# Optimization experiments

Measured on AMD Instinct MI355X. Metric: run time of the kernel, lower is better.

The kernel has to match this reference:

```python
import jax, jax.numpy as jnp
import numpy as np

BS, C_IN, CTX, TGT = 2, 8, 1024, 96
D_MODEL, N_HEADS, D_FF, N_LAYERS = 256, 16, 1024, 4
PF, SF, PC, SC = 8, 4, 32, 16
NF = (CTX + SF - PF) // SF + 1   # 256 fine patches (incl. end-pad)
NC = (CTX + SC - PC) // SC + 1   # 64 coarse patches
TOTAL = NF + NC                  # 320
EPS = 1e-5
DK = D_MODEL // N_HEADS
SCALE = DK ** -0.5


def _patchify(z, plen, stride):
    # ReplicationPad1d((0, stride)) then unfold -> (bs, c, n_patches, plen)
    pad = jnp.broadcast_to(z[..., -1:], z.shape[:-1] + (stride,))
    zp = jnp.concatenate([z, pad], axis=-1)
    n = (zp.shape[-1] - plen) // stride + 1
    idx = np.arange(n)[:, None] * stride + np.arange(plen)[None, :]
    return zp[..., idx]


def _layernorm(x, s, b):
    m = x.mean(-1, keepdims=True)
    v = jnp.var(x, axis=-1, keepdims=True)
    return (x - m) * jax.lax.rsqrt(v + EPS) * s + b


def setup_inputs() -> dict:
    key = jax.random.key(0)
    ks = jax.random.split(key, 16)
    g = lambda k, shape: jax.random.normal(k, shape, jnp.float32) * 0.02
    return {
        "z": jax.random.normal(ks[0], (BS, C_IN, CTX), jnp.float32),
        "revin_w": jnp.ones((C_IN,), jnp.float32),
        "revin_b": jnp.zeros((C_IN,), jnp.float32),
        "Wf": g(ks[1], (PF, D_MODEL)), "bf": jnp.zeros((D_MODEL,), jnp.float32),
        "Wc": g(ks[2], (PC, D_MODEL)), "bc": jnp.zeros((D_MODEL,), jnp.float32),
        "W_pos": jax.random.uniform(ks[3], (TOTAL, D_MODEL), jnp.float32, -0.02, 0.02),
        "WQ": g(ks[4], (N_LAYERS, D_MODEL, D_MODEL)), "bQ": jnp.zeros((N_LAYERS, D_MODEL), jnp.float32),
        "WK": g(ks[5], (N_LAYERS, D_MODEL, D_MODEL)), "bK": jnp.zeros((N_LAYERS, D_MODEL), jnp.float32),
        "WV": g(ks[6], (N_LAYERS, D_MODEL, D_MODEL)), "bV": jnp.zeros((N_LAYERS, D_MODEL), jnp.float32),
        "WO": g(ks[7], (N_LAYERS, D_MODEL, D_MODEL)), "bO": jnp.zeros((N_LAYERS, D_MODEL), jnp.float32),
        "ln1_s": jnp.ones((N_LAYERS, D_MODEL), jnp.float32), "ln1_b": jnp.zeros((N_LAYERS, D_MODEL), jnp.float32),
        "ln2_s": jnp.ones((N_LAYERS, D_MODEL), jnp.float32), "ln2_b": jnp.zeros((N_LAYERS, D_MODEL), jnp.float32),
        "F1": g(ks[8], (N_LAYERS, D_MODEL, D_FF)), "c1": jnp.zeros((N_LAYERS, D_FF), jnp.float32),
        "F2": g(ks[9], (N_LAYERS, D_FF, D_MODEL)), "c2": jnp.zeros((N_LAYERS, D_MODEL), jnp.float32),
        "Wh": g(ks[10], (D_MODEL * TOTAL, TGT)), "bh": jnp.zeros((TGT,), jnp.float32),
    }


def reference(z, revin_w, revin_b, Wf, bf, Wc, bc, W_pos, WQ, bQ, WK, bK, WV, bV,
              WO, bO, ln1_s, ln1_b, ln2_s, ln2_b, F1, c1, F2, c2, Wh, bh):
    # RevIN norm over the time axis (last axis of (bs, c, T))
    mean = z.mean(-1, keepdims=True)
    std = jnp.sqrt(jnp.var(z, axis=-1, keepdims=True) + EPS)
    zn = (z - mean) / std * revin_w[None, :, None] + revin_b[None, :, None]

    # dual-scale patch embedding
    x_fine = _patchify(zn, PF, SF) @ Wf + bf      # (bs, c, NF, d)
    x_coarse = _patchify(zn, PC, SC) @ Wc + bc    # (bs, c, NC, d)
    x = jnp.concatenate([x_fine, x_coarse], axis=2)  # (bs, c, TOTAL, d)

    u = x.reshape(BS * C_IN, TOTAL, D_MODEL) + W_pos  # (B, S, d), B=bs*c

    # residual-score transformer encoder (post-norm)
    prev = None
    for l in range(N_LAYERS):
        q = (u @ WQ[l] + bQ[l]).reshape(-1, TOTAL, N_HEADS, DK).transpose(0, 2, 1, 3)
        k = (u @ WK[l] + bK[l]).reshape(-1, TOTAL, N_HEADS, DK).transpose(0, 2, 1, 3)
        v = (u @ WV[l] + bV[l]).reshape(-1, TOTAL, N_HEADS, DK).transpose(0, 2, 1, 3)
        s = jnp.einsum('bhqd,bhkd->bhqk', q, k) * SCALE
        if prev is not None:
            s = s + prev
        w = jax.nn.softmax(s, axis=-1)
        o = jnp.einsum('bhqk,bhkd->bhqd', w, v).transpose(0, 2, 1, 3).reshape(-1, TOTAL, D_MODEL)
        o = o @ WO[l] + bO[l]
        u = _layernorm(u + o, ln1_s[l], ln1_b[l])
        h = jax.nn.gelu(u @ F1[l] + c1[l], approximate=False) @ F2[l] + c2[l]
        u = _layernorm(u + h, ln2_s[l], ln2_b[l])
        prev = s

    # head: (bs, c, TOTAL, d) -> permute -> flatten(d, TOTAL) -> linear
    zz = u.reshape(BS, C_IN, TOTAL, D_MODEL).transpose(0, 1, 3, 2).reshape(BS, C_IN, D_MODEL * TOTAL)
    out = zz @ Wh + bh  # (bs, c, TGT)

    # RevIN denorm
    out = (out - revin_b[None, :, None]) / (revin_w[None, :, None] + EPS * EPS) * std + mean
    return out
```

## Files before the change

kernel.cpp:

```cpp
#include <hip/hip_runtime.h>
#include <math.h>

typedef unsigned short ushort;
typedef unsigned int uint;
typedef __attribute__((ext_vector_type(8))) short short8;
typedef __attribute__((ext_vector_type(4))) float f32x4;
typedef __attribute__((ext_vector_type(4))) ushort us4;

constexpr int BS = 2, C_IN = 8, CTX = 1024, TGT = 96;
constexpr int DM = 256, NH = 16, DFF = 1024, NL = 4;
constexpr int NF = 256, TOTAL = 320;
constexpr int NB = 16;
constexpr int DK = 16;
constexpr float EPS = 1e-5f;
constexpr float SCALE = 0.25f;
constexpr int KHEAD = DM * TOTAL;
constexpr int M = NB * TOTAL;

__device__ __forceinline__ ushort f2b(float x) {
    uint u = __float_as_uint(x);
    u += 0x7fff + ((u >> 16) & 1);
    return (ushort)(u >> 16);
}
__device__ __forceinline__ float bu2f(ushort x) { return __uint_as_float(((uint)x) << 16); }
__device__ __forceinline__ uint pack2(float a, float b) { return (uint)f2b(a) | ((uint)f2b(b) << 16); }

typedef __attribute__((address_space(3))) uint lds_u32;
typedef const __attribute__((address_space(1))) uint glb_u32;
__device__ __forceinline__ void ldst16(const void* g, void* l) {
    __builtin_amdgcn_global_load_lds((glb_u32*)g, (lds_u32*)l, 16, 0, 0);
}

#define PIPE_BARRIER() asm volatile("s_waitcnt vmcnt(0)\n\ts_barrier" ::: "memory")

__global__ __launch_bounds__(256) void k_prep(
        const float* __restrict__ WQ, const float* __restrict__ WK,
        const float* __restrict__ WV, const float* __restrict__ WO,
        const float* __restrict__ F1, const float* __restrict__ F2,
        const float* __restrict__ Wh,
        ushort* __restrict__ Wtqkv, ushort* __restrict__ WtO,
        ushort* __restrict__ Ft1, ushort* __restrict__ Ft2,
        ushort* __restrict__ WhT2,
        const float* __restrict__ z, const float* __restrict__ rw,
        const float* __restrict__ rb,
        const float* __restrict__ Wf, const float* __restrict__ bfv,
        const float* __restrict__ Wc, const float* __restrict__ bcv,
        const float* __restrict__ Wpos, ushort* __restrict__ u,
        const float* __restrict__ bhv, float* __restrict__ outp,
        float* __restrict__ scalef) {
    __shared__ __align__(16) ushort tile[64 * 98];
    __shared__ float szn[CTX];
    __shared__ float red1[4], red2[4];
    int i = blockIdx.x, tid = threadIdx.x;

    if (i < 768) {
        const float* src; ushort* dst; int lsrc, ldst_, r0, c0;
        if (i < 256) {
            int mat = i >> 4, l = mat >> 2, w = mat & 3;
            src = (w == 0 ? WQ : (w == 1 ? WK : (w == 2 ? WV : WO))) + l * 65536;
            dst = (w < 3) ? (Wtqkv + (size_t)l * 768 * 256 + w * 65536)
                          : (WtO + (size_t)l * 65536);
            lsrc = 256; ldst_ = 256; r0 = ((i >> 2) & 3) * 64; c0 = (i & 3) * 64;
        } else if (i < 512) {
            int j = i - 256, l = j >> 6, t = j & 63;
            src = F1 + (size_t)l * 262144; dst = Ft1 + (size_t)l * 262144;
            lsrc = 1024; ldst_ = 256; r0 = (t >> 4) * 64; c0 = (t & 15) * 64;
        } else {
            int j = i - 512, l = j >> 6, t = j & 63;
            src = F2 + (size_t)l * 262144; dst = Ft2 + (size_t)l * 262144;
            lsrc = 256; ldst_ = 1024; r0 = (t >> 2) * 64; c0 = (t & 3) * 64;
        }
#pragma unroll
        for (int it = 0; it < 4; it++) {
            int fid = it * 256 + tid;
            int fr = fid >> 4, fc = fid & 15;
            f32x4 v = *(const f32x4*)&src[(size_t)(r0 + fr) * lsrc + c0 + fc * 4];
            ushort* tr = &tile[fr * 66];
            tr[fc * 4 + 0] = f2b(v[0]); tr[fc * 4 + 1] = f2b(v[1]);
            tr[fc * 4 + 2] = f2b(v[2]); tr[fc * 4 + 3] = f2b(v[3]);
        }
        __syncthreads();
#pragma unroll
        for (int it = 0; it < 4; it++) {
            int sid = it * 256 + tid;
            int cr = sid >> 4, cc = sid & 15;
            us4 v = (us4){ tile[(cc * 4 + 0) * 66 + cr], tile[(cc * 4 + 1) * 66 + cr],
                           tile[(cc * 4 + 2) * 66 + cr], tile[(cc * 4 + 3) * 66 + cr] };
            *(us4*)&dst[(size_t)(c0 + cr) * ldst_ + r0 + cc * 4] = v;
        }
    } else if (i < 2048) {
        int j = i - 768;
        int pp = j >> 2, d0 = (j & 3) * 64;
#pragma unroll
        for (int it = 0; it < 6; it++) {
            int fid = it * 256 + tid;
            int fr = fid / 24, fc = fid % 24;
            f32x4 v = *(const f32x4*)&Wh[((size_t)(d0 + fr) * 320 + pp) * 96 + fc * 4];
            ushort* tr = &tile[fr * 98];
            tr[fc * 4 + 0] = f2b(v[0]); tr[fc * 4 + 1] = f2b(v[1]);
            tr[fc * 4 + 2] = f2b(v[2]); tr[fc * 4 + 3] = f2b(v[3]);
        }
        __syncthreads();
#pragma unroll
        for (int it = 0; it < 6; it++) {
            int sid = it * 256 + tid;
            int tr = sid >> 4, dc = sid & 15;
            us4 v = (us4){ tile[(dc * 4 + 0) * 98 + tr], tile[(dc * 4 + 1) * 98 + tr],
                           tile[(dc * 4 + 2) * 98 + tr], tile[(dc * 4 + 3) * 98 + tr] };
            *(us4*)&WhT2[(size_t)tr * KHEAD + pp * 256 + d0 + dc * 4] = v;
        }
    } else {
        int j = i - 2048;
        int bc = j / 80, pb = j % 80;
        int wave = tid >> 6, lane = tid & 63;
        f32x4 zv = *(const f32x4*)&z[bc * CTX + tid * 4];
        float s1 = zv[0] + zv[1] + zv[2] + zv[3];
        float s2 = zv[0] * zv[0] + zv[1] * zv[1] + zv[2] * zv[2] + zv[3] * zv[3];
#pragma unroll
        for (int off = 1; off < 64; off <<= 1) {
            s1 += __shfl_xor(s1, off);
            s2 += __shfl_xor(s2, off);
        }
        if (lane == 0) { red1[wave] = s1; red2[wave] = s2; }
        __syncthreads();
        s1 = red1[0] + red1[1] + red1[2] + red1[3];
        s2 = red2[0] + red2[1] + red2[2] + red2[3];
        float m = s1 * (1.0f / CTX);
        float var = s2 * (1.0f / CTX) - m * m;
        float sd = sqrtf(var + EPS);
        int c = bc & 7;
        float w = rw[c], bb = rb[c];
        float inv_sd_w = w / sd;
#pragma unroll
        for (int k = 0; k < 4; k++) szn[tid * 4 + k] = (zv[k] - m) * inv_sd_w + bb;
        if (pb == 0) {
            if (tid < TGT) outp[bc * TGT + tid] = (bhv[tid] - bb) / (w + EPS * EPS) * sd + m;
            if (tid == 0) scalef[bc] = sd / (w + EPS * EPS);
        }
        __syncthreads();
#pragma unroll
        for (int pi = 0; pi < 4; pi++) {
            int p = pb * 4 + pi, d = tid;
            float acc;
            if (p < NF) {
                acc = bfv[d];
                int base = p * 4;
#pragma unroll
                for (int q = 0; q < 8; q++)
                    acc += szn[min(base + q, CTX - 1)] * Wf[q * DM + d];
            } else {
                acc = bcv[d];
                int base = (p - NF) * 16;
#pragma unroll
                for (int q = 0; q < 32; q++)
                    acc += szn[min(base + q, CTX - 1)] * Wc[q * DM + d];
            }
            acc += Wpos[p * DM + d];
            u[((size_t)bc * TOTAL + p) * DM + d] = f2b(acc);
        }
    }
}

template <int GELU, int QKV>
__global__ __launch_bounds__(256) void k_gemm_mfma(const ushort* __restrict__ A,
                                                   const ushort* __restrict__ Wt,
                                                   const float* __restrict__ b0,
                                                   const float* __restrict__ b1,
                                                   const float* __restrict__ b2,
                                                   ushort* __restrict__ C,
                                                   ushort* __restrict__ C2,
                                                   int Mm, int N, int K) {
    __shared__ ushort As[2][64][32];
    __shared__ ushort Bs[2][64][32];
    int tid = threadIdx.x;
    int wave = tid >> 6, lane = tid & 63;
    int quad = lane >> 4, l16 = lane & 15;
    int m0 = blockIdx.y * 64, n0 = blockIdx.x * 64;

    f32x4 acc[4];
#pragma unroll
    for (int nt = 0; nt < 4; nt++) acc[nt] = (f32x4){0.f, 0.f, 0.f, 0.f};

    int srow = wave * 16 + (lane >> 2);
    int sc = (lane & 3) ^ ((srow >> 1) & 3);
    const ushort* Ag = &A[(size_t)(m0 + srow) * K + sc * 8];
    const ushort* Bg = &Wt[(size_t)(n0 + srow) * K + sc * 8];
    int rchunk = (quad ^ ((l16 >> 1) & 3)) * 8;

    ldst16(Ag, &As[0][wave * 16][0]);
    ldst16(Bg, &Bs[0][wave * 16][0]);
    PIPE_BARRIER();

    int nstep = K >> 5;
    int cur = 0;
    for (int t = 0; t < nstep; t++) {
        if (t + 1 < nstep) {
            ldst16(Ag + (t + 1) * 32, &As[cur ^ 1][wave * 16][0]);
            ldst16(Bg + (t + 1) * 32, &Bs[cur ^ 1][wave * 16][0]);
        }
        short8 af = *(const short8*)&As[cur][wave * 16 + l16][rchunk];
#pragma unroll
        for (int nt = 0; nt < 4; nt++) {
            short8 bf = *(const short8*)&Bs[cur][nt * 16 + l16][rchunk];
            acc[nt] = __builtin_amdgcn_mfma_f32_16x16x32_bf16(af, bf, acc[nt], 0, 0, 0);
        }
        PIPE_BARRIER();
        cur ^= 1;
    }
#pragma unroll
    for (int nt = 0; nt < 4; nt++) {
        int col = n0 + nt * 16 + l16;
        float bi;
        if (QKV) {
            int bs = (n0 + nt * 16) >> 8;
            const float* bp = bs == 0 ? b0 : (bs == 1 ? b1 : b2);
            bi = bp[col & 255];
        } else {
            bi = b0[col];
        }
#pragma unroll
        for (int r = 0; r < 4; r++) {
            int rowm = m0 + wave * 16 + quad * 4 + r;
            float vv = acc[nt][r] + bi;
            if (GELU) vv = vv * 0.5f * (1.0f + erff(vv * 0.70710678118f));
            if (QKV) {
                int bs = col >> 8;
                ushort* dst = (bs == 2) ? (C2 + (size_t)rowm * DM)
                                        : (C + (size_t)bs * (M * DM) + (size_t)rowm * DM);
                dst[col & 255] = f2b(vv);
            } else {
                C[(size_t)rowm * N + col] = f2b(vv);
            }
        }
    }
}

__global__ __launch_bounds__(256) void k_gemm_ln16(const ushort* __restrict__ A,
                                                   const ushort* __restrict__ Wt,
                                                   const float* __restrict__ bias,
                                                   const float* __restrict__ ls,
                                                   const float* __restrict__ lb,
                                                   ushort* __restrict__ u, int K) {
    __shared__ ushort As[2][16][32];
    __shared__ ushort Bs[2][256][32];
    __shared__ float ps1[16][4], ps2[16][4];
    int tid = threadIdx.x;
    int wave = tid >> 6, lane = tid & 63;
    int quad = lane >> 4, l16 = lane & 15;
    int m0 = blockIdx.x * 16;

    f32x4 acc[4];
#pragma unroll
    for (int nt = 0; nt < 4; nt++) acc[nt] = (f32x4){0.f, 0.f, 0.f, 0.f};

    int brow = wave * 16 + (lane >> 2);
    int bc_swz = (lane & 3) ^ ((brow >> 1) & 3);
    const ushort* Bg0 = &Wt[(size_t)brow * K + bc_swz * 8];
    int ar = lane >> 2;
    int ac = (lane & 3) ^ ((ar >> 1) & 3);
    const ushort* Ag = &A[(size_t)(m0 + ar) * K + ac * 8];
    int rchunk = (quad ^ ((l16 >> 1) & 3)) * 8;

    if (tid < 64) ldst16(Ag, &As[0][0][0]);
#pragma unroll
    for (int i = 0; i < 4; i++)
        ldst16(Bg0 + (size_t)i * 64 * K, &Bs[0][i * 64 + wave * 16][0]);
    PIPE_BARRIER();

    int nstep = K >> 5;
    int cur = 0;
    for (int t = 0; t < nstep; t++) {
        if (t + 1 < nstep) {
            if (tid < 64) ldst16(Ag + (t + 1) * 32, &As[cur ^ 1][0][0]);
#pragma unroll
            for (int i = 0; i < 4; i++)
                ldst16(Bg0 + (size_t)i * 64 * K + (t + 1) * 32, &Bs[cur ^ 1][i * 64 + wave * 16][0]);
        }
        short8 af = *(const short8*)&As[cur][l16][rchunk];
#pragma unroll
        for (int nt = 0; nt < 4; nt++) {
            short8 bf = *(const short8*)&Bs[cur][wave * 64 + nt * 16 + l16][rchunk];
            acc[nt] = __builtin_amdgcn_mfma_f32_16x16x32_bf16(af, bf, acc[nt], 0, 0, 0);
        }
        PIPE_BARRIER();
        cur ^= 1;
    }
    float xv[4][4];
#pragma unroll
    for (int r = 0; r < 4; r++) {
        int rowg = m0 + quad * 4 + r;
        float s1 = 0.f, s2 = 0.f;
#pragma unroll
        for (int nt = 0; nt < 4; nt++) {
            int col = wave * 64 + nt * 16 + l16;
            float x = acc[nt][r] + bias[col] + bu2f(u[(size_t)rowg * DM + col]);
            xv[r][nt] = x; s1 += x; s2 += x * x;
        }
        s1 += __shfl_xor(s1, 1); s2 += __shfl_xor(s2, 1);
        s1 += __shfl_xor(s1, 2); s2 += __shfl_xor(s2, 2);
        s1 += __shfl_xor(s1, 4); s2 += __shfl_xor(s2, 4);
        s1 += __shfl_xor(s1, 8); s2 += __shfl_xor(s2, 8);
        if (l16 == 0) { ps1[quad * 4 + r][wave] = s1; ps2[quad * 4 + r][wave] = s2; }
    }
    __syncthreads();
#pragma unroll
    for (int r = 0; r < 4; r++) {
        int rowl = quad * 4 + r, rowg = m0 + rowl;
        float s1 = ps1[rowl][0] + ps1[rowl][1] + ps1[rowl][2] + ps1[rowl][3];
        float s2 = ps2[rowl][0] + ps2[rowl][1] + ps2[rowl][2] + ps2[rowl][3];
        float m = s1 * (1.0f / DM);
        float var = s2 * (1.0f / DM) - m * m;
        float rs = rsqrtf(var + EPS);
#pragma unroll
        for (int nt = 0; nt < 4; nt++) {
            int col = wave * 64 + nt * 16 + l16;
            u[(size_t)rowg * DM + col] = f2b((xv[r][nt] - m) * rs * ls[col] + lb[col]);
        }
    }
}

__global__ __launch_bounds__(256, 4) void k_attn(const ushort* __restrict__ qk, const ushort* __restrict__ vm,
                                                 ushort* __restrict__ ao, int nj) {
    __shared__ ushort sh[15360];
    uint* sh32 = (uint*)sh;
    int bh = blockIdx.x, b = bh >> 4, h = bh & 15;
    int i0 = blockIdx.y * 64;
    int t = threadIdx.x, wave = t >> 6, lane = t & 63, quad = lane >> 4, l16 = lane & 15;
    const short8 zero8 = (short8){0, 0, 0, 0, 0, 0, 0, 0};

    f32x4 acc[20];
#pragma unroll
    for (int nt = 0; nt < 20; nt++) acc[nt] = (f32x4){0.f, 0.f, 0.f, 0.f};

    for (int idx = t; idx < 320; idx += 256) {
        int jp = idx >> 1, dh = idx & 1;
        int j = jp * 2;
        uint4 a = *(const uint4*)&vm[((size_t)b * TOTAL + j) * DM + h * DK + dh * 8];
        uint4 bb = *(const uint4*)&vm[((size_t)b * TOTAL + j + 1) * DM + h * DK + dh * 8];
        const ushort* ap = (const ushort*)&a;
        const ushort* bp = (const ushort*)&bb;
        int jr = j & 31;
        int q = (jr & 15) >> 2, jj = ((jr >> 4) << 2) + (jr & 3);
        int base = 10240 + ((j >> 5) * 4 + q) * 128 + jj;
#pragma unroll
        for (int dd = 0; dd < 8; dd++) {
            int d = dh * 8 + dd;
            uint val = (uint)ap[dd] | ((uint)bp[dd] << 16);
            sh32[(base + d * 8) >> 1] = val;
        }
    }

    for (int jl = 0; jl < nj; jl++) {
        const ushort* qm = qk + (size_t)(2 * jl) * M * DM;
        const ushort* km = qm + (size_t)M * DM;
        int kb = (jl & 1) * 5120;
        for (int idx = t; idx < 640; idx += 256) {
            int j = idx >> 1, half = idx & 1;
            short8 kv = *(const short8*)&km[((size_t)b * TOTAL + j) * DM + h * DK + half * 8];
            int jt = j >> 4, jln = j & 15;
            *(short8*)&sh[kb + ((jt * 2 + half) * 16 + jln) * 8] = kv;
        }
        short8 qf = zero8;
        if (quad < 2) qf = *(const short8*)&qm[((size_t)b * TOTAL + i0 + wave * 16 + l16) * DM + h * DK + quad * 8];
        __syncthreads();
#pragma unroll
        for (int nt = 0; nt < 20; nt++) {
            short8 kf = *(const short8*)&sh[kb + ((nt * 2 + (quad & 1)) * 16 + l16) * 8];
            acc[nt] = __builtin_amdgcn_mfma_f32_16x16x32_bf16(kf, qf, acc[nt], 0, 0, 0);
        }
    }

    float mx = -1e30f;
#pragma unroll
    for (int nt = 0; nt < 20; nt++)
#pragma unroll
        for (int r = 0; r < 4; r++) { acc[nt][r] *= SCALE; mx = fmaxf(mx, acc[nt][r]); }
    mx = fmaxf(mx, __shfl_xor(mx, 16));
    mx = fmaxf(mx, __shfl_xor(mx, 32));
    float sum = 0.f;
#pragma unroll
    for (int nt = 0; nt < 20; nt++)
#pragma unroll
        for (int r = 0; r < 4; r++) { acc[nt][r] = __expf(acc[nt][r] - mx); sum += acc[nt][r]; }
    sum += __shfl_xor(sum, 16);
    sum += __shfl_xor(sum, 32);
    float inv = 1.f / sum;
#pragma unroll
    for (int nt = 0; nt < 20; nt++)
#pragma unroll
        for (int r = 0; r < 4; r++) acc[nt][r] *= inv;

    f32x4 oacc = (f32x4){0.f, 0.f, 0.f, 0.f};
#pragma unroll
    for (int jt2 = 0; jt2 < 10; jt2++) {
        short8 vt = *(const short8*)&sh[10240 + ((jt2 * 4 + quad) * 16 + l16) * 8];
        union { short8 v; uint u[4]; } pf;
        pf.u[0] = pack2(acc[2 * jt2][0], acc[2 * jt2][1]);
        pf.u[1] = pack2(acc[2 * jt2][2], acc[2 * jt2][3]);
        pf.u[2] = pack2(acc[2 * jt2 + 1][0], acc[2 * jt2 + 1][1]);
        pf.u[3] = pack2(acc[2 * jt2 + 1][2], acc[2 * jt2 + 1][3]);
        oacc = __builtin_amdgcn_mfma_f32_16x16x32_bf16(vt, pf.v, oacc, 0, 0, 0);
    }
    us4 ov4 = (us4){f2b(oacc[0]), f2b(oacc[1]), f2b(oacc[2]), f2b(oacc[3])};
    *(us4*)&ao[((size_t)b * TOTAL + i0 + wave * 16 + l16) * DM + h * DK + quad * 4] = ov4;
}

__global__ __launch_bounds__(256) void k_head(const ushort* __restrict__ u, const ushort* __restrict__ WhT2,
                                              const float* __restrict__ scalef, float* __restrict__ out) {
    int t0 = blockIdx.x * 16;
    int wave = threadIdx.x >> 6, lane = threadIdx.x & 63;
    int quad = lane >> 4, l16 = lane & 15;
    int chunk = blockIdx.y * 4 + wave;
    int kbeg = chunk * 1024;
    f32x4 acc = (f32x4){0.f, 0.f, 0.f, 0.f};
    const ushort* za = &u[(size_t)l16 * KHEAD + quad * 8];
    const ushort* wb = &WhT2[(size_t)(t0 + l16) * KHEAD + quad * 8];
#pragma unroll 4
    for (int k = kbeg; k < kbeg + 1024; k += 32) {
        short8 af = *(const short8*)&za[k];
        short8 bf = *(const short8*)&wb[k];
        acc = __builtin_amdgcn_mfma_f32_16x16x32_bf16(af, bf, acc, 0, 0, 0);
    }
#pragma unroll
    for (int r = 0; r < 4; r++) {
        int bcr = quad * 4 + r;
        atomicAdd(&out[bcr * TGT + t0 + l16], acc[r] * scalef[bcr]);
    }
}

extern "C" void kernel_launch(void* const* d_in, const int* in_sizes, int n_in,
                              void* d_out, int out_size, void* d_ws, size_t ws_size,
                              hipStream_t stream) {
    const float* z       = (const float*)d_in[0];
    const float* revin_w = (const float*)d_in[1];
    const float* revin_b = (const float*)d_in[2];
    const float* Wf      = (const float*)d_in[3];
    const float* bfv     = (const float*)d_in[4];
    const float* Wc      = (const float*)d_in[5];
    const float* bcv     = (const float*)d_in[6];
    const float* Wpos    = (const float*)d_in[7];
    const float* WQ      = (const float*)d_in[8];
    const float* bQ      = (const float*)d_in[9];
    const float* WK      = (const float*)d_in[10];
    const float* bK      = (const float*)d_in[11];
    const float* WV      = (const float*)d_in[12];
    const float* bV      = (const float*)d_in[13];
    const float* WO      = (const float*)d_in[14];
    const float* bO      = (const float*)d_in[15];
    const float* ln1s    = (const float*)d_in[16];
    const float* ln1b    = (const float*)d_in[17];
    const float* ln2s    = (const float*)d_in[18];
    const float* ln2b    = (const float*)d_in[19];
    const float* F1      = (const float*)d_in[20];
    const float* c1      = (const float*)d_in[21];
    const float* F2      = (const float*)d_in[22];
    const float* c2      = (const float*)d_in[23];
    const float* Wh      = (const float*)d_in[24];
    const float* bh      = (const float*)d_in[25];
    float* out = (float*)d_out;

    char* p = (char*)d_ws;
    float* scalef = (float*)p;   p += 16 * 4;
    p = (char*)(((size_t)p + 255) & ~255ull);
    ushort* u     = (ushort*)p;  p += (size_t)M * DM * 2;
    ushort* qkbuf = (ushort*)p;  p += (size_t)NL * 2 * M * DM * 2;
    ushort* vbuf  = (ushort*)p;  p += (size_t)M * DM * 2;
    ushort* ax    = (ushort*)p;  p += (size_t)M * DM * 2;
    ushort* hbuf  = (ushort*)p;  p += (size_t)M * DFF * 2;
    ushort* Wtqkv = (ushort*)p;  p += (size_t)NL * 768 * 256 * 2;
    ushort* WtO   = (ushort*)p;  p += (size_t)NL * 256 * 256 * 2;
    ushort* Ft1   = (ushort*)p;  p += (size_t)NL * 1024 * 256 * 2;
    ushort* Ft2   = (ushort*)p;  p += (size_t)NL * 256 * 1024 * 2;
    ushort* WhT2  = (ushort*)p;  p += (size_t)TGT * KHEAD * 2;

    k_prep<<<3328, 256, 0, stream>>>(WQ, WK, WV, WO, F1, F2, Wh,
                                     Wtqkv, WtO, Ft1, Ft2, WhT2,
                                     z, revin_w, revin_b,
                                     Wf, bfv, Wc, bcv, Wpos, u,
                                     bh, out, scalef);

    for (int l = 0; l < NL; l++) {
        k_gemm_mfma<0, 1><<<dim3(12, 80), 256, 0, stream>>>(
            u, Wtqkv + (size_t)l * 768 * 256, bQ + l * DM, bK + l * DM, bV + l * DM,
            qkbuf + (size_t)l * 2 * M * DM, vbuf, M, 768, 256);
        k_attn<<<dim3(NB * NH, 5), 256, 0, stream>>>(qkbuf, vbuf, ax, l + 1);
        k_gemm_ln16<<<M / 16, 256, 0, stream>>>(
            ax, WtO + (size_t)l * 65536, bO + l * DM, ln1s + l * DM, ln1b + l * DM, u, 256);
        k_gemm_mfma<1, 0><<<dim3(16, 80), 256, 0, stream>>>(
            u, Ft1 + (size_t)l * 262144, c1 + l * DFF, c1, c1, hbuf, hbuf, M, 1024, 256);
        k_gemm_ln16<<<M / 16, 256, 0, stream>>>(
            hbuf, Ft2 + (size_t)l * 262144, c2 + l * DM, ln2s + l * DM, ln2b + l * DM, u, 1024);
    }

    k_head<<<dim3(TGT / 16, 20), 256, 0, stream>>>(u, WhT2, scalef, out);
}
```

Baseline: 441.4 us.

## Triple-buffer LDS in MFMA GEMM kernels with partial vmcnt waits

Both the generic MFMA GEMM and the GEMM+LayerNorm kernel move from double to triple-buffered LDS staging. Loads run two K-steps ahead, and the wait at each step uses a partial vmcnt count instead of draining every outstanding load. This hides more global-load latency behind the MFMAs. In exchange it uses more LDS per block, and it relies on exact vmcnt counts per wave, which differ for wave 0 because it issues the extra A loads.

```diff
diff --git a/kernel.cpp b/kernel.cpp
--- a/kernel.cpp
+++ b/kernel.cpp
@@ -31,7 +31,9 @@
     __builtin_amdgcn_global_load_lds((glb_u32*)g, (lds_u32*)l, 16, 0, 0);
 }
 
-#define PIPE_BARRIER() asm volatile("s_waitcnt vmcnt(0)\n\ts_barrier" ::: "memory")
+#define WAITV(n) asm volatile("s_waitcnt vmcnt(" #n ")" ::: "memory")
+#define SBAR()   asm volatile("s_barrier" ::: "memory")
+#define SBARW()  asm volatile("s_waitcnt lgkmcnt(0)\n\ts_barrier" ::: "memory")
 
 __global__ __launch_bounds__(256) void k_prep(
         const float* __restrict__ WQ, const float* __restrict__ WK,
@@ -170,8 +172,8 @@
                                                    ushort* __restrict__ C,
                                                    ushort* __restrict__ C2,
                                                    int Mm, int N, int K) {
-    __shared__ ushort As[2][64][32];
-    __shared__ ushort Bs[2][64][32];
+    __shared__ ushort As[3][64][32];
+    __shared__ ushort Bs[3][64][32];
     int tid = threadIdx.x;
     int wave = tid >> 6, lane = tid & 63;
     int quad = lane >> 4, l16 = lane & 15;
@@ -187,25 +189,32 @@
     const ushort* Bg = &Wt[(size_t)(n0 + srow) * K + sc * 8];
     int rchunk = (quad ^ ((l16 >> 1) & 3)) * 8;
 
-    ldst16(Ag, &As[0][wave * 16][0]);
-    ldst16(Bg, &Bs[0][wave * 16][0]);
-    PIPE_BARRIER();
-
     int nstep = K >> 5;
+    ldst16(Ag,      &As[0][wave * 16][0]);
+    ldst16(Bg,      &Bs[0][wave * 16][0]);
+    ldst16(Ag + 32, &As[1][wave * 16][0]);
+    ldst16(Bg + 32, &Bs[1][wave * 16][0]);
+    ldst16(Ag + 64, &As[2][wave * 16][0]);
+    ldst16(Bg + 64, &Bs[2][wave * 16][0]);
+
     int cur = 0;
     for (int t = 0; t < nstep; t++) {
-        if (t + 1 < nstep) {
-            ldst16(Ag + (t + 1) * 32, &As[cur ^ 1][wave * 16][0]);
-            ldst16(Bg + (t + 1) * 32, &Bs[cur ^ 1][wave * 16][0]);
-        }
+        if (t < nstep - 2) WAITV(4);
+        else if (t == nstep - 2) WAITV(2);
+        else WAITV(0);
+        SBAR();
         short8 af = *(const short8*)&As[cur][wave * 16 + l16][rchunk];
 #pragma unroll
         for (int nt = 0; nt < 4; nt++) {
             short8 bf = *(const short8*)&Bs[cur][nt * 16 + l16][rchunk];
             acc[nt] = __builtin_amdgcn_mfma_f32_16x16x32_bf16(af, bf, acc[nt], 0, 0, 0);
         }
-        PIPE_BARRIER();
-        cur ^= 1;
+        if (t + 3 < nstep) {
+            SBARW();
+            ldst16(Ag + (t + 3) * 32, &As[cur][wave * 16][0]);
+            ldst16(Bg + (t + 3) * 32, &Bs[cur][wave * 16][0]);
+        }
+        cur = (cur == 2) ? 0 : cur + 1;
     }
 #pragma unroll
     for (int nt = 0; nt < 4; nt++) {
@@ -241,8 +250,8 @@
                                                    const float* __restrict__ ls,
                                                    const float* __restrict__ lb,
                                                    ushort* __restrict__ u, int K) {
-    __shared__ ushort As[2][16][32];
-    __shared__ ushort Bs[2][256][32];
+    __shared__ ushort As[3][16][32];
+    __shared__ ushort Bs[3][256][32];
     __shared__ float ps1[16][4], ps2[16][4];
     int tid = threadIdx.x;
     int wave = tid >> 6, lane = tid & 63;
@@ -261,29 +270,41 @@
     const ushort* Ag = &A[(size_t)(m0 + ar) * K + ac * 8];
     int rchunk = (quad ^ ((l16 >> 1) & 3)) * 8;
 
+    int nstep = K >> 5;
     if (tid < 64) ldst16(Ag, &As[0][0][0]);
 #pragma unroll
-    for (int i = 0; i < 4; i++)
-        ldst16(Bg0 + (size_t)i * 64 * K, &Bs[0][i * 64 + wave * 16][0]);
-    PIPE_BARRIER();
-
-    int nstep = K >> 5;
+    for (int i = 0; i < 4; i++) ldst16(Bg0 + (size_t)i * 64 * K, &Bs[0][i * 64 + wave * 16][0]);
+    if (tid < 64) ldst16(Ag + 32, &As[1][0][0]);
+#pragma unroll
+    for (int i = 0; i < 4; i++) ldst16(Bg0 + (size_t)i * 64 * K + 32, &Bs[1][i * 64 + wave * 16][0]);
+    if (tid < 64) ldst16(Ag + 64, &As[2][0][0]);
+#pragma unroll
+    for (int i = 0; i < 4; i++) ldst16(Bg0 + (size_t)i * 64 * K + 64, &Bs[2][i * 64 + wave * 16][0]);
+
     int cur = 0;
     for (int t = 0; t < nstep; t++) {
-        if (t + 1 < nstep) {
-            if (tid < 64) ldst16(Ag + (t + 1) * 32, &As[cur ^ 1][0][0]);
-#pragma unroll
-            for (int i = 0; i < 4; i++)
-                ldst16(Bg0 + (size_t)i * 64 * K + (t + 1) * 32, &Bs[cur ^ 1][i * 64 + wave * 16][0]);
-        }
+        if (t < nstep - 2) {
+            if (wave == 0) WAITV(10); else WAITV(8);
+        } else if (t == nstep - 2) {
+            if (wave == 0) WAITV(5); else WAITV(4);
+        } else {
+            WAITV(0);
+        }
+        SBAR();
         short8 af = *(const short8*)&As[cur][l16][rchunk];
 #pragma unroll
         for (int nt = 0; nt < 4; nt++) {
             short8 bf = *(const short8*)&Bs[cur][wave * 64 + nt * 16 + l16][rchunk];
             acc[nt] = __builtin_amdgcn_mfma_f32_16x16x32_bf16(af, bf, acc[nt], 0, 0, 0);
         }
-        PIPE_BARRIER();
-        cur ^= 1;
+        if (t + 3 < nstep) {
+            SBARW();
+            if (tid < 64) ldst16(Ag + (t + 3) * 32, &As[cur][0][0]);
+#pragma unroll
+            for (int i = 0; i < 4; i++)
+                ldst16(Bg0 + (size_t)i * 64 * K + (t + 3) * 32, &Bs[cur][i * 64 + wave * 16][0]);
+        }
+        cur = (cur == 2) ? 0 : cur + 1;
     }
     float xv[4][4];
 #pragma unroll
```

Measured after the change: 440.0 us. Within noise of the previous version (-0.3%).

## Fuse FFN up-projection, GELU, down-projection and LayerNorm into one kernel

Applied to the files above, without the earlier changes.

Replaces the separate FFN1 GEMM and the FFN2+LayerNorm GEMM with a single kernel. Each block processes 16 rows and keeps the 16x1024 GELU activations in shared memory, so the hidden buffer no longer makes a round trip through global memory and one launch per layer is removed. Weights are now read straight from global memory with no LDS staging, so every block re-reads the full F1 and F2 matrices. This relies on L2 for reuse and has long dependent MFMA chains with little latency hiding.

```diff
diff --git a/kernel.cpp b/kernel.cpp
--- a/kernel.cpp
+++ b/kernel.cpp
@@ -294,6 +294,105 @@
         for (int nt = 0; nt < 4; nt++) {
             int col = wave * 64 + nt * 16 + l16;
             float x = acc[nt][r] + bias[col] + bu2f(u[(size_t)rowg * DM + col]);
+            xv[r][nt] = x; s1 += x; s2 += x * x;
+        }
+        s1 += __shfl_xor(s1, 1); s2 += __shfl_xor(s2, 1);
+        s1 += __shfl_xor(s1, 2); s2 += __shfl_xor(s2, 2);
+        s1 += __shfl_xor(s1, 4); s2 += __shfl_xor(s2, 4);
+        s1 += __shfl_xor(s1, 8); s2 += __shfl_xor(s2, 8);
+        if (l16 == 0) { ps1[quad * 4 + r][wave] = s1; ps2[quad * 4 + r][wave] = s2; }
+    }
+    __syncthreads();
+#pragma unroll
+    for (int r = 0; r < 4; r++) {
+        int rowl = quad * 4 + r, rowg = m0 + rowl;
+        float s1 = ps1[rowl][0] + ps1[rowl][1] + ps1[rowl][2] + ps1[rowl][3];
+        float s2 = ps2[rowl][0] + ps2[rowl][1] + ps2[rowl][2] + ps2[rowl][3];
+        float m = s1 * (1.0f / DM);
+        float var = s2 * (1.0f / DM) - m * m;
+        float rs = rsqrtf(var + EPS);
+#pragma unroll
+        for (int nt = 0; nt < 4; nt++) {
+            int col = wave * 64 + nt * 16 + l16;
+            u[(size_t)rowg * DM + col] = f2b((xv[r][nt] - m) * rs * ls[col] + lb[col]);
+        }
+    }
+}
+
+__global__ __launch_bounds__(256) void k_ffn(const ushort* __restrict__ u_in,
+                                             const ushort* __restrict__ F1t,
+                                             const ushort* __restrict__ F2t,
+                                             const float* __restrict__ c1v,
+                                             const float* __restrict__ c2v,
+                                             const float* __restrict__ ls,
+                                             const float* __restrict__ lb,
+                                             ushort* __restrict__ u) {
+    __shared__ __align__(16) ushort Au[16][264];
+    __shared__ __align__(16) ushort Hs[16][1032];
+    __shared__ float ps1[16][4], ps2[16][4];
+    int tid = threadIdx.x;
+    int wave = tid >> 6, lane = tid & 63;
+    int quad = lane >> 4, l16 = lane & 15;
+    int m0 = blockIdx.x * 16;
+
+    for (int s = tid; s < 512; s += 256) {
+        int row = s >> 5, k32 = (s >> 2) & 7, pp = s & 3;
+        int logical = pp ^ ((row >> 1) & 3);
+        short8 v = *(const short8*)&u_in[(size_t)(m0 + row) * DM + k32 * 32 + logical * 8];
+        *(short8*)&Au[row][k32 * 32 + pp * 8] = v;
+    }
+    __syncthreads();
+
+    int rchunk = (quad ^ ((l16 >> 1) & 3)) * 8;
+
+    for (int ct = 0; ct < 16; ct++) {
+        f32x4 acc = (f32x4){0.f, 0.f, 0.f, 0.f};
+        int coln = wave * 256 + ct * 16 + l16;
+        const ushort* brow = &F1t[(size_t)coln * DM + quad * 8];
+#pragma unroll
+        for (int t = 0; t < 8; t++) {
+            short8 af = *(const short8*)&Au[l16][t * 32 + rchunk];
+            short8 bf = *(const short8*)&brow[t * 32];
+            acc = __builtin_amdgcn_mfma_f32_16x16x32_bf16(af, bf, acc, 0, 0, 0);
+        }
+        int k32 = coln >> 5, p = (coln >> 3) & 3, e = coln & 7;
+        float bi = c1v[coln];
+#pragma unroll
+        for (int r = 0; r < 4; r++) {
+            int row = quad * 4 + r;
+            float vv = acc[r] + bi;
+            vv = vv * 0.5f * (1.0f + erff(vv * 0.70710678118f));
+            int pphys = p ^ ((row >> 1) & 3);
+            Hs[row][k32 * 32 + pphys * 8 + e] = f2b(vv);
+        }
+    }
+    __syncthreads();
+
+    f32x4 acc[4];
+#pragma unroll
+    for (int nt = 0; nt < 4; nt++) acc[nt] = (f32x4){0.f, 0.f, 0.f, 0.f};
+#pragma unroll 2
+    for (int t = 0; t < 32; t++) {
+        short8 af = *(const short8*)&Hs[l16][t * 32 + rchunk];
+#pragma unroll
+        for (int nt = 0; nt < 4; nt++) {
+            int coln = wave * 64 + nt * 16 + l16;
+            short8 bf = *(const short8*)&F2t[(size_t)coln * DFF + t * 32 + quad * 8];
+            acc[nt] = __builtin_amdgcn_mfma_f32_16x16x32_bf16(af, bf, acc[nt], 0, 0, 0);
+        }
+    }
+
+    float xv[4][4];
+#pragma unroll
+    for (int r = 0; r < 4; r++) {
+        int row = quad * 4 + r;
+        float s1 = 0.f, s2 = 0.f;
+#pragma unroll
+        for (int nt = 0; nt < 4; nt++) {
+            int col = wave * 64 + nt * 16 + l16;
+            int k32 = col >> 5, p = (col >> 3) & 3, e = col & 7;
+            int pphys = p ^ ((row >> 1) & 3);
+            float x = acc[nt][r] + c2v[col] + bu2f(Au[row][k32 * 32 + pphys * 8 + e]);
             xv[r][nt] = x; s1 += x; s2 += x * x;
         }
         s1 += __shfl_xor(s1, 1); s2 += __shfl_xor(s2, 1);
@@ -466,7 +565,6 @@
     ushort* qkbuf = (ushort*)p;  p += (size_t)NL * 2 * M * DM * 2;
     ushort* vbuf  = (ushort*)p;  p += (size_t)M * DM * 2;
     ushort* ax    = (ushort*)p;  p += (size_t)M * DM * 2;
-    ushort* hbuf  = (ushort*)p;  p += (size_t)M * DFF * 2;
     ushort* Wtqkv = (ushort*)p;  p += (size_t)NL * 768 * 256 * 2;
     ushort* WtO   = (ushort*)p;  p += (size_t)NL * 256 * 256 * 2;
     ushort* Ft1   = (ushort*)p;  p += (size_t)NL * 1024 * 256 * 2;
@@ -486,10 +584,9 @@
         k_attn<<<dim3(NB * NH, 5), 256, 0, stream>>>(qkbuf, vbuf, ax, l + 1);
         k_gemm_ln16<<<M / 16, 256, 0, stream>>>(
             ax, WtO + (size_t)l * 65536, bO + l * DM, ln1s + l * DM, ln1b + l * DM, u, 256);
-        k_gemm_mfma<1, 0><<<dim3(16, 80), 256, 0, stream>>>(
-            u, Ft1 + (size_t)l * 262144, c1 + l * DFF, c1, c1, hbuf, hbuf, M, 1024, 256);
-        k_gemm_ln16<<<M / 16, 256, 0, stream>>>(
-            hbuf, Ft2 + (size_t)l * 262144, c2 + l * DM, ln2s + l * DM, ln2b + l * DM, u, 1024);
+        k_ffn<<<M / 16, 256, 0, stream>>>(
+            u, Ft1 + (size_t)l * 262144, Ft2 + (size_t)l * 262144,
+            c1 + l * DFF, c2 + l * DM, ln2s + l * DM, ln2b + l * DM, u);
     }
 
     k_head<<<dim3(TGT / 16, 20), 256, 0, stream>>>(u, WhT2, scalef, out);
```

Result: slower. 542.8 us (+23.0%).
